# Kernel optimization log

Measured on AMD Instinct MI355X. Metric: run time of the kernel, lower is better.

Reference implementation:

```python
import jax, jax.numpy as jnp
import numpy as np
import math

B, N, D = 4096, 196, 32
M, H, W, NH = 12, 14, 14, 4
DH = D // NH


def _coords():
    # k_coords: (N,2) grid coords; q_coords: first M points of a (sqrt(M)+1)^2 linspace grid
    yy, xx = np.meshgrid(np.arange(H), np.arange(W), indexing='ij')
    k_coords = np.stack([yy.ravel(), xx.ravel()], axis=-1).astype(np.float32)
    g = int(math.sqrt(M)) + 1  # 4
    cy = np.linspace(0, H - 1, g)
    cx = np.linspace(0, W - 1, g)
    gy, gx = np.meshgrid(cy, cx, indexing='ij')
    grid = np.stack([gy.ravel(), gx.ravel()], axis=-1).astype(np.float32)
    q_coords = grid[:M]
    return jnp.asarray(q_coords), jnp.asarray(k_coords)


def setup_inputs() -> dict:
    key = jax.random.key(0)
    ks = jax.random.split(key, 8)
    q_coords, k_coords = _coords()
    return {
        'T': jax.random.normal(ks[0], (B, N, D), jnp.float32),
        'Q': jax.random.normal(ks[1], (M, D), jnp.float32) * 0.02,
        'Wq': jax.random.normal(ks[2], (D, D), jnp.float32) / math.sqrt(D),
        'Wk': jax.random.normal(ks[3], (D, D), jnp.float32) / math.sqrt(D),
        'Wv': jax.random.normal(ks[4], (D, D), jnp.float32) / math.sqrt(D),
        'Wp': jax.random.normal(ks[5], (D, M * D), jnp.float32) / math.sqrt(M * D),
        'bp': jnp.zeros((D,), jnp.float32),
        'rpb_bias': jax.random.normal(ks[6], (NH, 2 * H - 1, 2 * W - 1), jnp.float32) * 0.02,
        'q_coords': q_coords,
        'k_coords': k_coords,
    }


def reference(T, Q, Wq, Wk, Wv, Wp, bp, rpb_bias, q_coords, k_coords):
    # projections (torch Linear: x @ W^T)
    Qp = Q @ Wq.T                      # (M, D)
    K = T @ Wk.T                       # (B, N, D)
    V = T @ Wv.T                       # (B, N, D)
    Qh = Qp.reshape(M, NH, DH).transpose(1, 0, 2)          # (nh, M, Dh)
    Kh = K.reshape(B, N, NH, DH).transpose(0, 2, 1, 3)     # (B, nh, N, Dh)
    Vh = V.reshape(B, N, NH, DH).transpose(0, 2, 1, 3)     # (B, nh, N, Dh)

    content = jnp.einsum('hmd,bhnd->bhmn', Qh, Kh) / math.sqrt(DH)

    # gathered relative position bias: (nh, M, N)
    dy = q_coords[:, None, 0] - k_coords[None, :, 0]
    dx = q_coords[:, None, 1] - k_coords[None, :, 1]
    idx_y = jnp.clip(jnp.round(dy) + (H - 1), 0, 2 * H - 2).astype(jnp.int32)
    idx_x = jnp.clip(jnp.round(dx) + (W - 1), 0, 2 * W - 2).astype(jnp.int32)
    rpb = rpb_bias[:, idx_y, idx_x]

    logits = content + rpb[None]                            # (B, nh, M, N)
    A = jax.nn.softmax(logits, axis=-1)

    A_avg = A.mean(axis=1)                                  # (B, M, N)
    topk = max(1, int(0.05 * N))                            # 9
    topk_mass = jax.lax.top_k(A_avg, topk)[0].sum(-1)       # (B, M)

    P = jnp.clip(A, 1e-12, None)
    Hn = -(P * jnp.log(P)).sum(-1) / math.log(N)            # (B, nh, M)
    head_energy = (1.0 - Hn).transpose(0, 2, 1)             # (B, M, nh)

    S = jnp.einsum('bhmn,bhnd->bhmd', A, Vh).transpose(0, 2, 1, 3).reshape(B, M, D)
    Z = S.reshape(B, M * D) @ Wp.T + bp                     # (B, D)
    A_maps = A_avg.reshape(B, M, H, W)
    return Z, A_maps, head_energy, S, topk_mass
```

## Files before the change

kernel.cpp:

```cpp
#include <hip/hip_runtime.h>
#include <math.h>


typedef float f32x4 __attribute__((ext_vector_type(4)));
typedef float f32x2 __attribute__((ext_vector_type(2)));
typedef _Float16 h2  __attribute__((ext_vector_type(2)));
typedef _Float16 h4v __attribute__((ext_vector_type(4)));
typedef _Float16 h8  __attribute__((ext_vector_type(8)));
typedef __fp16 fp16x2 __attribute__((ext_vector_type(2)));

#define LOG2E 1.4426950408889634f

__device__ __forceinline__ h2 cvt_pk(float a, float b){
  fp16x2 r = __builtin_amdgcn_cvt_pkrtz(a, b);
  return __builtin_bit_cast(h2, r);
}

__device__ __forceinline__ float dot4(float4 a, float4 b){
  return a.x*b.x + a.y*b.y + a.z*b.z + a.w*b.w;
}

__device__ __forceinline__ void barrier_lds(){
  asm volatile("s_waitcnt lgkmcnt(0)" ::: "memory");
  __builtin_amdgcn_s_barrier();
  asm volatile("" ::: "memory");
}

template<int CTRL>
__device__ __forceinline__ int idpp(int x, int id){
  return __builtin_amdgcn_update_dpp(id, x, CTRL, 0xF, 0xF, false);
}
__device__ __forceinline__ int wimax_all(int x){
  const int ID = 0;
  x = max(x, idpp<0x111>(x, ID));
  x = max(x, idpp<0x112>(x, ID));
  x = max(x, idpp<0x114>(x, ID));
  x = max(x, idpp<0x118>(x, ID));
  x = max(x, idpp<0x142>(x, ID));
  x = max(x, idpp<0x143>(x, ID));
  return __builtin_amdgcn_readlane(x, 63);
}

__global__ void prologue_kernel(const float* __restrict__ Q, const float* __restrict__ Wq,
                                const float* __restrict__ Wk, const float* __restrict__ Wv,
                                const float* __restrict__ rpb,
                                const float* __restrict__ qc, const float* __restrict__ kc,
                                _Float16* __restrict__ G16, float* __restrict__ rpbc32,
                                float* __restrict__ Wvp)
{
  __shared__ float Qp[384];
  const int tid = threadIdx.x;
  const int bid = blockIdx.x;

  if (bid == 0){
    for (int i = tid; i < 384; i += 256){
      int m = i >> 5, d = i & 31;
      float a = 0.f;
      #pragma unroll
      for (int c = 0; c < 32; ++c) a += Q[m*32+c] * Wq[d*32+c];
      Qp[i] = a;
    }
    __syncthreads();
    const float s = 0.35355339059327373f * LOG2E;
    for (int i = tid; i < 1536; i += 256){
      int hm = i >> 5, c = i & 31;
      int hh = hm / 12, mm = hm - 12*hh;
      float a = 0.f;
      #pragma unroll
      for (int dh = 0; dh < 8; ++dh) a += Qp[mm*32 + hh*8 + dh] * Wk[(hh*8+dh)*32 + c];
      G16[i] = (_Float16)(a * s);
    }
  }
  if (bid == 1){
    for (int i = tid; i < 1024; i += 256){
      int d = i >> 5, cp = i & 31;
      Wvp[i] = Wv[d*32 + (cp>>1) + ((cp&1)<<4)];
    }
  }
  int i = bid*256 + tid;
  if (i < 9984){
    int mh = i / 208, n = i - mh*208;
    float v;
    if (n < 196){
      int hh = mh / 12, mm = mh - 12*hh;
      float dy = qc[2*mm]   - kc[2*n];
      float dx = qc[2*mm+1] - kc[2*n+1];
      int iy = (int)rintf(dy) + 13; iy = iy < 0 ? 0 : (iy > 26 ? 26 : iy);
      int ix = (int)rintf(dx) + 13; ix = ix < 0 ? 0 : (ix > 26 ? 26 : ix);
      v = rpb[hh*729 + iy*27 + ix];
    } else {
      v = -60000.0f;
    }
    rpbc32[i] = v * LOG2E;
  }
}

__device__ __forceinline__ int ttoff(int n, int c8){
  return (n>>2)*128 + ((c8>>1)<<6) + ((n&3)<<4) + ((c8&1)<<3);
}

#define TRRD(dst, base, off) \
  asm volatile("ds_read_b64_tr_b16 %0, %1 offset:" #off : "=v"(dst) : "v"(base))
#define SH8(a, b) __builtin_shufflevector(a, b, 0,1,2,3,4,5,6,7)

__global__ __launch_bounds__(256, 4) void fused_main(
    const float* __restrict__ T, const float* __restrict__ Wvp, const float* __restrict__ Wp,
    const float* __restrict__ bp, const _Float16* __restrict__ G16,
    const float* __restrict__ rpbc32, float* __restrict__ out)
{
  __shared__ __align__(128) char smem[39456];
  _Float16* TT = (_Float16*)smem;
  _Float16* As = (_Float16*)(smem + 13312);
  float*    U  = (float*)(smem + 32544);
  float*    Ss = (float*)smem;

  const int b    = blockIdx.x;
  const int tid  = threadIdx.x;
  const int lane = tid & 63;
  const int h    = tid >> 6;
  const int r15  = lane & 15;
  const int g    = lane >> 4;

  float* outZ = out;
  float* outA = out + 131072;
  float* outE = out + 9764864;
  float* outS = out + 9961472;
  float* outK = out + 11534336;

  const float* Tb = T + (size_t)b*6272;
  #pragma unroll
  for (int ii = 0; ii < 3; ++ii){
    int i = tid + ii*256;
    int n = i >> 2, c8 = i & 3;
    const f32x4* src = (const f32x4*)(Tb + n*32 + c8*8);
    f32x4 v0 = __builtin_nontemporal_load(src);
    f32x4 v1 = __builtin_nontemporal_load(src + 1);
    h2 p0 = cvt_pk(v0[0], v0[1]);
    h2 p1 = cvt_pk(v0[2], v0[3]);
    h2 p2 = cvt_pk(v1[0], v1[1]);
    h2 p3 = cvt_pk(v1[2], v1[3]);
    h4v lo = __builtin_shufflevector(p0, p1, 0,1,2,3);
    h4v hi = __builtin_shufflevector(p2, p3, 0,1,2,3);
    *(h8*)&TT[ttoff(n, c8)] = __builtin_shufflevector(lo, hi, 0,1,2,3,4,5,6,7);
  }
  if (tid < 64){
    int i = 768 + tid;
    int n = i >> 2, c8 = i & 3;
    h8 hv = {0,0,0,0,0,0,0,0};
    if (n < 196){
      const f32x4* src = (const f32x4*)(Tb + n*32 + c8*8);
      f32x4 v0 = __builtin_nontemporal_load(src);
      f32x4 v1 = __builtin_nontemporal_load(src + 1);
      h2 p0 = cvt_pk(v0[0], v0[1]);
      h2 p1 = cvt_pk(v0[2], v0[3]);
      h2 p2 = cvt_pk(v1[0], v1[1]);
      h2 p3 = cvt_pk(v1[2], v1[3]);
      h4v lo = __builtin_shufflevector(p0, p1, 0,1,2,3);
      h4v hi = __builtin_shufflevector(p2, p3, 0,1,2,3);
      hv = __builtin_shufflevector(lo, hi, 0,1,2,3,4,5,6,7);
    }
    *(h8*)&TT[ttoff(n, c8)] = hv;
  }
  if (tid < 2){
    h8 z = {0,0,0,0,0,0,0,0};
    *(h8*)&As[9600 + tid*8] = z;
  }

  const int mhB = h*12 + (r15 < 12 ? r15 : 11);
  h8 bfrag = *(const h8*)(G16 + mhB*32 + g*8);
  f32x4 acc[13];
  #pragma unroll
  for (int t = 0; t < 13; ++t)
    acc[t] = *(const f32x4*)(rpbc32 + mhB*208 + t*16 + g*4);
  barrier_lds();

  const int rowoff = ((r15>>2)*128) + ((r15&3)<<4) + ((g>>1)<<6) + ((g&1)<<3);
  #pragma unroll
  for (int t = 0; t < 13; ++t){
    h8 af = *(const h8*)&TT[rowoff + t*512];
    acc[t] = __builtin_amdgcn_mfma_f32_16x16x32_f16(af, bfrag, acc[t], 0, 0, 0);
  }

  float se = 0.f, te = 0.f;
  #pragma unroll
  for (int t = 0; t < 13; ++t){
    #pragma unroll
    for (int r = 0; r < 4; ++r){
      float x = acc[t][r];
      float e = __builtin_amdgcn_exp2f(x);
      se += e; te += x*e;
      acc[t][r] = e;
    }
  }
  se += __shfl_xor(se, 16); se += __shfl_xor(se, 32);
  te += __shfl_xor(te, 16); te += __shfl_xor(te, 32);
  const float inv = 1.f / se;
  if (r15 < 12){
    #pragma unroll
    for (int t = 0; t < 13; ++t){
      if (t == 12){
        if (g >= 2) continue;
      }
      h2 w0 = cvt_pk(acc[t][0]*inv, acc[t][1]*inv);
      h2 w1 = cvt_pk(acc[t][2]*inv, acc[t][3]*inv);
      *(h4v*)&As[mhB*200 + t*16 + g*4] = __builtin_shufflevector(w0, w1, 0,1,2,3);
    }
    if (g == 0){
      const float LOG2N_INV = 0.13132474f;
      outE[(size_t)b*48 + r15*4 + h] = 1.0f + (te*inv - __log2f(se)) * LOG2N_INV;
    }
  }
  barrier_lds();

  if (h < 3){
    f32x4 u0 = {0,0,0,0}, u1 = {0,0,0,0};
    const int arow = h*16 + r15;
    const _Float16* Ab = &As[arow*200 + g*8];
    h8 af0 = *(const h8*)(Ab);
    h8 af1 = *(const h8*)(Ab + 32);
    h8 af2 = *(const h8*)(Ab + 64);
    h8 af3 = *(const h8*)(Ab + 96);
    h8 af4 = *(const h8*)(Ab + 128);
    h8 af5 = *(const h8*)(Ab + 160);
    h4v afT = *(const h4v*)&As[arow*200 + 192 + g*4];
    unsigned A0 = (unsigned)(size_t)&TT[0] + (unsigned)(g*512 + r15*8);
    unsigned At = (unsigned)(size_t)&TT[0] + (unsigned)(12288 + g*256 + r15*8);
    h4v t00,t01,t02,t03, t10,t11,t12,t13, t20,t21,t22,t23,
        t30,t31,t32,t33, t40,t41,t42,t43, t50,t51,t52,t53, tt0,tt1;
    TRRD(t00, A0, 0);     TRRD(t01, A0, 256);   TRRD(t02, A0, 128);   TRRD(t03, A0, 384);
    TRRD(t10, A0, 2048);  TRRD(t11, A0, 2304);  TRRD(t12, A0, 2176);  TRRD(t13, A0, 2432);
    TRRD(t20, A0, 4096);  TRRD(t21, A0, 4352);  TRRD(t22, A0, 4224);  TRRD(t23, A0, 4480);
    TRRD(t30, A0, 6144);  TRRD(t31, A0, 6400);  TRRD(t32, A0, 6272);  TRRD(t33, A0, 6528);
    TRRD(t40, A0, 8192);  TRRD(t41, A0, 8448);  TRRD(t42, A0, 8320);  TRRD(t43, A0, 8576);
    TRRD(t50, A0, 10240); TRRD(t51, A0, 10496); TRRD(t52, A0, 10368); TRRD(t53, A0, 10624);
    TRRD(tt0, At, 0);     TRRD(tt1, At, 128);
    asm volatile("s_waitcnt lgkmcnt(0)" ::: "memory");
    __builtin_amdgcn_sched_barrier(0);
    u0 = __builtin_amdgcn_mfma_f32_16x16x32_f16(af0, SH8(t00,t01), u0, 0, 0, 0);
    u1 = __builtin_amdgcn_mfma_f32_16x16x32_f16(af0, SH8(t02,t03), u1, 0, 0, 0);
    u0 = __builtin_amdgcn_mfma_f32_16x16x32_f16(af1, SH8(t10,t11), u0, 0, 0, 0);
    u1 = __builtin_amdgcn_mfma_f32_16x16x32_f16(af1, SH8(t12,t13), u1, 0, 0, 0);
    u0 = __builtin_amdgcn_mfma_f32_16x16x32_f16(af2, SH8(t20,t21), u0, 0, 0, 0);
    u1 = __builtin_amdgcn_mfma_f32_16x16x32_f16(af2, SH8(t22,t23), u1, 0, 0, 0);
    u0 = __builtin_amdgcn_mfma_f32_16x16x32_f16(af3, SH8(t30,t31), u0, 0, 0, 0);
    u1 = __builtin_amdgcn_mfma_f32_16x16x32_f16(af3, SH8(t32,t33), u1, 0, 0, 0);
    u0 = __builtin_amdgcn_mfma_f32_16x16x32_f16(af4, SH8(t40,t41), u0, 0, 0, 0);
    u1 = __builtin_amdgcn_mfma_f32_16x16x32_f16(af4, SH8(t42,t43), u1, 0, 0, 0);
    u0 = __builtin_amdgcn_mfma_f32_16x16x32_f16(af5, SH8(t50,t51), u0, 0, 0, 0);
    u1 = __builtin_amdgcn_mfma_f32_16x16x32_f16(af5, SH8(t52,t53), u1, 0, 0, 0);
    u0 = __builtin_amdgcn_mfma_f32_16x16x16f16(afT, tt0, u0, 0, 0, 0);
    u1 = __builtin_amdgcn_mfma_f32_16x16x16f16(afT, tt1, u1, 0, 0, 0);
    #pragma unroll
    for (int r = 0; r < 4; ++r){
      f32x2 p = {u0[r], u1[r]};
      *(f32x2*)&U[(h*16 + g*4 + r)*36 + r15*2] = p;
    }
  }

  {
    const bool act = (lane < 49);
    const int nb4 = lane * 4;
    int K00=0,K01=0,K02=0,K03=0, K10=0,K11=0,K12=0,K13=0, K20=0,K21=0,K22=0,K23=0;
    float mass0=0.f, mass1=0.f, mass2=0.f;
    const int m0 = h, m1 = h+4, m2 = h+8;

    #pragma unroll
    for (int mi = 0; mi < 3; ++mi){
      int m = (mi==0) ? m0 : ((mi==1) ? m1 : m2);
      if (act){
        h4v s0 = *(const h4v*)&As[(     m)*200 + nb4];
        h4v s1 = *(const h4v*)&As[(12 + m)*200 + nb4];
        h4v s2 = *(const h4v*)&As[(24 + m)*200 + nb4];
        h4v s3 = *(const h4v*)&As[(36 + m)*200 + nb4];
        h4v sh = (s0 + s1) + (s2 + s3);
        float a0 = 0.25f*(float)sh[0], a1 = 0.25f*(float)sh[1];
        float a2 = 0.25f*(float)sh[2], a3 = 0.25f*(float)sh[3];
        float* amrow = outA + (size_t)b*2352 + m*196 + nb4;
        f32x2 o0 = {a0, a1}, o1 = {a2, a3};
        __builtin_nontemporal_store(o0, (f32x2*)amrow);
        __builtin_nontemporal_store(o1, (f32x2*)(amrow + 2));
        int kk0 = (__builtin_bit_cast(int, a0) & ~0xFF) | (lane << 2) | 0;
        int kk1 = (__builtin_bit_cast(int, a1) & ~0xFF) | (lane << 2) | 1;
        int kk2 = (__builtin_bit_cast(int, a2) & ~0xFF) | (lane << 2) | 2;
        int kk3 = (__builtin_bit_cast(int, a3) & ~0xFF) | (lane << 2) | 3;
        if (mi == 0){ K00=kk0; K01=kk1; K02=kk2; K03=kk3; }
        else if (mi == 1){ K10=kk0; K11=kk1; K12=kk2; K13=kk3; }
        else { K20=kk0; K21=kk1; K22=kk2; K23=kk3; }
      }
    }
    #pragma unroll
    for (int k = 0; k < 9; ++k){
      int g0 = wimax_all(max(max(K00,K01), max(K02,K03)));
      int g1 = wimax_all(max(max(K10,K11), max(K12,K13)));
      int g2 = wimax_all(max(max(K20,K21), max(K22,K23)));
      mass0 += __builtin_bit_cast(float, g0 & ~0xFF);
      mass1 += __builtin_bit_cast(float, g1 & ~0xFF);
      mass2 += __builtin_bit_cast(float, g2 & ~0xFF);
      if (lane == ((g0 >> 2) & 63)){
        int q = g0 & 3;
        if (q==0) K00=0; else if (q==1) K01=0; else if (q==2) K02=0; else K03=0;
      }
      if (lane == ((g1 >> 2) & 63)){
        int q = g1 & 3;
        if (q==0) K10=0; else if (q==1) K11=0; else if (q==2) K12=0; else K13=0;
      }
      if (lane == ((g2 >> 2) & 63)){
        int q = g2 & 3;
        if (q==0) K20=0; else if (q==1) K21=0; else if (q==2) K22=0; else K23=0;
      }
    }
    if (lane == 0){
      __builtin_nontemporal_store(mass0, outK + (size_t)b*12 + m0);
      __builtin_nontemporal_store(mass1, outK + (size_t)b*12 + m1);
      __builtin_nontemporal_store(mass2, outK + (size_t)b*12 + m2);
    }
  }
  barrier_lds();

  for (int md = tid; md < 384; md += 256){
    int m = md >> 5, d = md & 31, hh = d >> 3;
    const float4* Urow = (const float4*)(U + (hh*12 + m)*36);
    const float4* Wvr  = (const float4*)(Wvp + d*32);
    float a = 0.f;
    #pragma unroll
    for (int q = 0; q < 8; ++q) a += dot4(Urow[q], Wvr[q]);
    Ss[md] = a;
    __builtin_nontemporal_store(a, outS + (size_t)b*384 + md);
  }
  barrier_lds();

  {
    int d = tid >> 3, j4 = tid & 7;
    const float4* Wp4 = (const float4*)(Wp + d*384);
    const float4* Ss4 = (const float4*)Ss;
    float a = 0.f;
    #pragma unroll
    for (int jj = 0; jj < 12; ++jj){
      int j = j4 + jj*8;
      a += dot4(Wp4[j], Ss4[j]);
    }
    a += __shfl_xor(a, 1);
    a += __shfl_xor(a, 2);
    a += __shfl_xor(a, 4);
    if (j4 == 0)
      __builtin_nontemporal_store(bp[d] + a, outZ + (size_t)b*32 + d);
  }
}

extern "C" void kernel_launch(void* const* d_in, const int* in_sizes, int n_in,
                              void* d_out, int out_size, void* d_ws, size_t ws_size,
                              hipStream_t stream)
{
  const float* T    = (const float*)d_in[0];
  const float* Q    = (const float*)d_in[1];
  const float* Wq   = (const float*)d_in[2];
  const float* Wk   = (const float*)d_in[3];
  const float* Wv   = (const float*)d_in[4];
  const float* Wp   = (const float*)d_in[5];
  const float* bp   = (const float*)d_in[6];
  const float* rpb  = (const float*)d_in[7];
  const float* qc   = (const float*)d_in[8];
  const float* kc   = (const float*)d_in[9];
  _Float16* G16  = (_Float16*)d_ws;
  float* rpbc32  = (float*)((char*)d_ws + 4096);
  float* Wvp     = (float*)((char*)d_ws + 44032);
  float* outp = (float*)d_out;

  prologue_kernel<<<40, 256, 0, stream>>>(Q, Wq, Wk, Wv, rpb, qc, kc, G16, rpbc32, Wvp);
  fused_main<<<4096, 256, 0, stream>>>(T, Wvp, Wp, bp, G16, rpbc32, outp);
}
```

Before: 69.37 us.

## Make fused kernel persistent over four batches with register-prefetched next tile

The grid shrinks from one block per batch to 1024 blocks, each looping over four batch elements. During each iteration the next batch's T tile is loaded from global memory into registers while the top-k and output phases run, then packed into LDS after a barrier. Ss moves to a separate LDS region so it does not collide with the TT tile being refilled. This aims to hide global load latency and amortize block launch, but it raises register pressure and gives fewer blocks to balance across CUs.

After: 198.4 us. 2.86x slower.

```diff
diff --git a/kernel.cpp b/kernel.cpp
--- a/kernel.cpp
+++ b/kernel.cpp
@@ -10,10 +10,19 @@
 typedef __fp16 fp16x2 __attribute__((ext_vector_type(2)));
 
 #define LOG2E 1.4426950408889634f
+#define GRIDB 1024
+#define NB    4
 
 __device__ __forceinline__ h2 cvt_pk(float a, float b){
   fp16x2 r = __builtin_amdgcn_cvt_pkrtz(a, b);
   return __builtin_bit_cast(h2, r);
+}
+__device__ __forceinline__ h8 pack8(f32x4 a, f32x4 b){
+  h2 q0 = cvt_pk(a[0],a[1]), q1 = cvt_pk(a[2],a[3]);
+  h2 q2 = cvt_pk(b[0],b[1]), q3 = cvt_pk(b[2],b[3]);
+  h4v lo = __builtin_shufflevector(q0,q1,0,1,2,3);
+  h4v hi = __builtin_shufflevector(q2,q3,0,1,2,3);
+  return __builtin_shufflevector(lo,hi,0,1,2,3,4,5,6,7);
 }
 
 __device__ __forceinline__ float dot4(float4 a, float4 b){
@@ -112,9 +121,9 @@
   _Float16* TT = (_Float16*)smem;
   _Float16* As = (_Float16*)(smem + 13312);
   float*    U  = (float*)(smem + 32544);
-  float*    Ss = (float*)smem;
-
-  const int b    = blockIdx.x;
+  float*    Ss = (float*)(smem + 13312);
+
+  const int bid  = blockIdx.x;
   const int tid  = threadIdx.x;
   const int lane = tid & 63;
   const int h    = tid >> 6;
@@ -127,39 +136,28 @@
   float* outS = out + 9961472;
   float* outK = out + 11534336;
 
-  const float* Tb = T + (size_t)b*6272;
-  #pragma unroll
-  for (int ii = 0; ii < 3; ++ii){
-    int i = tid + ii*256;
-    int n = i >> 2, c8 = i & 3;
-    const f32x4* src = (const f32x4*)(Tb + n*32 + c8*8);
-    f32x4 v0 = __builtin_nontemporal_load(src);
-    f32x4 v1 = __builtin_nontemporal_load(src + 1);
-    h2 p0 = cvt_pk(v0[0], v0[1]);
-    h2 p1 = cvt_pk(v0[2], v0[3]);
-    h2 p2 = cvt_pk(v1[0], v1[1]);
-    h2 p3 = cvt_pk(v1[2], v1[3]);
-    h4v lo = __builtin_shufflevector(p0, p1, 0,1,2,3);
-    h4v hi = __builtin_shufflevector(p2, p3, 0,1,2,3);
-    *(h8*)&TT[ttoff(n, c8)] = __builtin_shufflevector(lo, hi, 0,1,2,3,4,5,6,7);
-  }
-  if (tid < 64){
-    int i = 768 + tid;
-    int n = i >> 2, c8 = i & 3;
-    h8 hv = {0,0,0,0,0,0,0,0};
-    if (n < 196){
-      const f32x4* src = (const f32x4*)(Tb + n*32 + c8*8);
+  {
+    const float* Tb = T + (size_t)bid*6272;
+    #pragma unroll
+    for (int ii = 0; ii < 3; ++ii){
+      int i = tid + ii*256;
+      const f32x4* src = (const f32x4*)(Tb + (i>>2)*32 + (i&3)*8);
       f32x4 v0 = __builtin_nontemporal_load(src);
       f32x4 v1 = __builtin_nontemporal_load(src + 1);
-      h2 p0 = cvt_pk(v0[0], v0[1]);
-      h2 p1 = cvt_pk(v0[2], v0[3]);
-      h2 p2 = cvt_pk(v1[0], v1[1]);
-      h2 p3 = cvt_pk(v1[2], v1[3]);
-      h4v lo = __builtin_shufflevector(p0, p1, 0,1,2,3);
-      h4v hi = __builtin_shufflevector(p2, p3, 0,1,2,3);
-      hv = __builtin_shufflevector(lo, hi, 0,1,2,3,4,5,6,7);
-    }
-    *(h8*)&TT[ttoff(n, c8)] = hv;
+      *(h8*)&TT[ttoff(i>>2, i&3)] = pack8(v0, v1);
+    }
+    if (tid < 64){
+      int i = 768 + tid;
+      int n = i >> 2;
+      h8 hv = {0,0,0,0,0,0,0,0};
+      if (n < 196){
+        const f32x4* src = (const f32x4*)(Tb + n*32 + (i&3)*8);
+        f32x4 v0 = __builtin_nontemporal_load(src);
+        f32x4 v1 = __builtin_nontemporal_load(src + 1);
+        hv = pack8(v0, v1);
+      }
+      *(h8*)&TT[ttoff(n, i&3)] = hv;
+    }
   }
   if (tid < 2){
     h8 z = {0,0,0,0,0,0,0,0};
@@ -167,183 +165,230 @@
   }
 
   const int mhB = h*12 + (r15 < 12 ? r15 : 11);
-  h8 bfrag = *(const h8*)(G16 + mhB*32 + g*8);
+  const h8 bfrag = *(const h8*)(G16 + mhB*32 + g*8);
   f32x4 acc[13];
   #pragma unroll
   for (int t = 0; t < 13; ++t)
     acc[t] = *(const f32x4*)(rpbc32 + mhB*208 + t*16 + g*4);
-  barrier_lds();
 
   const int rowoff = ((r15>>2)*128) + ((r15&3)<<4) + ((g>>1)<<6) + ((g&1)<<3);
-  #pragma unroll
-  for (int t = 0; t < 13; ++t){
-    h8 af = *(const h8*)&TT[rowoff + t*512];
-    acc[t] = __builtin_amdgcn_mfma_f32_16x16x32_f16(af, bfrag, acc[t], 0, 0, 0);
-  }
-
-  float se = 0.f, te = 0.f;
-  #pragma unroll
-  for (int t = 0; t < 13; ++t){
-    #pragma unroll
-    for (int r = 0; r < 4; ++r){
-      float x = acc[t][r];
-      float e = __builtin_amdgcn_exp2f(x);
-      se += e; te += x*e;
-      acc[t][r] = e;
-    }
-  }
-  se += __shfl_xor(se, 16); se += __shfl_xor(se, 32);
-  te += __shfl_xor(te, 16); te += __shfl_xor(te, 32);
-  const float inv = 1.f / se;
-  if (r15 < 12){
+
+  for (int it = 0; it < NB; ++it){
+    const int b = bid + it*GRIDB;
+    barrier_lds();
+
     #pragma unroll
     for (int t = 0; t < 13; ++t){
-      if (t == 12){
-        if (g >= 2) continue;
-      }
-      h2 w0 = cvt_pk(acc[t][0]*inv, acc[t][1]*inv);
-      h2 w1 = cvt_pk(acc[t][2]*inv, acc[t][3]*inv);
-      *(h4v*)&As[mhB*200 + t*16 + g*4] = __builtin_shufflevector(w0, w1, 0,1,2,3);
-    }
-    if (g == 0){
-      const float LOG2N_INV = 0.13132474f;
-      outE[(size_t)b*48 + r15*4 + h] = 1.0f + (te*inv - __log2f(se)) * LOG2N_INV;
-    }
-  }
-  barrier_lds();
-
-  if (h < 3){
-    f32x4 u0 = {0,0,0,0}, u1 = {0,0,0,0};
-    const int arow = h*16 + r15;
-    const _Float16* Ab = &As[arow*200 + g*8];
-    h8 af0 = *(const h8*)(Ab);
-    h8 af1 = *(const h8*)(Ab + 32);
-    h8 af2 = *(const h8*)(Ab + 64);
-    h8 af3 = *(const h8*)(Ab + 96);
-    h8 af4 = *(const h8*)(Ab + 128);
-    h8 af5 = *(const h8*)(Ab + 160);
-    h4v afT = *(const h4v*)&As[arow*200 + 192 + g*4];
-    unsigned A0 = (unsigned)(size_t)&TT[0] + (unsigned)(g*512 + r15*8);
-    unsigned At = (unsigned)(size_t)&TT[0] + (unsigned)(12288 + g*256 + r15*8);
-    h4v t00,t01,t02,t03, t10,t11,t12,t13, t20,t21,t22,t23,
-        t30,t31,t32,t33, t40,t41,t42,t43, t50,t51,t52,t53, tt0,tt1;
-    TRRD(t00, A0, 0);     TRRD(t01, A0, 256);   TRRD(t02, A0, 128);   TRRD(t03, A0, 384);
-    TRRD(t10, A0, 2048);  TRRD(t11, A0, 2304);  TRRD(t12, A0, 2176);  TRRD(t13, A0, 2432);
-    TRRD(t20, A0, 4096);  TRRD(t21, A0, 4352);  TRRD(t22, A0, 4224);  TRRD(t23, A0, 4480);
-    TRRD(t30, A0, 6144);  TRRD(t31, A0, 6400);  TRRD(t32, A0, 6272);  TRRD(t33, A0, 6528);
-    TRRD(t40, A0, 8192);  TRRD(t41, A0, 8448);  TRRD(t42, A0, 8320);  TRRD(t43, A0, 8576);
-    TRRD(t50, A0, 10240); TRRD(t51, A0, 10496); TRRD(t52, A0, 10368); TRRD(t53, A0, 10624);
-    TRRD(tt0, At, 0);     TRRD(tt1, At, 128);
-    asm volatile("s_waitcnt lgkmcnt(0)" ::: "memory");
-    __builtin_amdgcn_sched_barrier(0);
-    u0 = __builtin_amdgcn_mfma_f32_16x16x32_f16(af0, SH8(t00,t01), u0, 0, 0, 0);
-    u1 = __builtin_amdgcn_mfma_f32_16x16x32_f16(af0, SH8(t02,t03), u1, 0, 0, 0);
-    u0 = __builtin_amdgcn_mfma_f32_16x16x32_f16(af1, SH8(t10,t11), u0, 0, 0, 0);
-    u1 = __builtin_amdgcn_mfma_f32_16x16x32_f16(af1, SH8(t12,t13), u1, 0, 0, 0);
-    u0 = __builtin_amdgcn_mfma_f32_16x16x32_f16(af2, SH8(t20,t21), u0, 0, 0, 0);
-    u1 = __builtin_amdgcn_mfma_f32_16x16x32_f16(af2, SH8(t22,t23), u1, 0, 0, 0);
-    u0 = __builtin_amdgcn_mfma_f32_16x16x32_f16(af3, SH8(t30,t31), u0, 0, 0, 0);
-    u1 = __builtin_amdgcn_mfma_f32_16x16x32_f16(af3, SH8(t32,t33), u1, 0, 0, 0);
-    u0 = __builtin_amdgcn_mfma_f32_16x16x32_f16(af4, SH8(t40,t41), u0, 0, 0, 0);
-    u1 = __builtin_amdgcn_mfma_f32_16x16x32_f16(af4, SH8(t42,t43), u1, 0, 0, 0);
-    u0 = __builtin_amdgcn_mfma_f32_16x16x32_f16(af5, SH8(t50,t51), u0, 0, 0, 0);
-    u1 = __builtin_amdgcn_mfma_f32_16x16x32_f16(af5, SH8(t52,t53), u1, 0, 0, 0);
-    u0 = __builtin_amdgcn_mfma_f32_16x16x16f16(afT, tt0, u0, 0, 0, 0);
-    u1 = __builtin_amdgcn_mfma_f32_16x16x16f16(afT, tt1, u1, 0, 0, 0);
+      h8 af = *(const h8*)&TT[rowoff + t*512];
+      acc[t] = __builtin_amdgcn_mfma_f32_16x16x32_f16(af, bfrag, acc[t], 0, 0, 0);
+    }
+
+    float se = 0.f, te = 0.f;
     #pragma unroll
-    for (int r = 0; r < 4; ++r){
-      f32x2 p = {u0[r], u1[r]};
-      *(f32x2*)&U[(h*16 + g*4 + r)*36 + r15*2] = p;
-    }
-  }
-
-  {
-    const bool act = (lane < 49);
-    const int nb4 = lane * 4;
-    int K00=0,K01=0,K02=0,K03=0, K10=0,K11=0,K12=0,K13=0, K20=0,K21=0,K22=0,K23=0;
-    float mass0=0.f, mass1=0.f, mass2=0.f;
-    const int m0 = h, m1 = h+4, m2 = h+8;
-
-    #pragma unroll
-    for (int mi = 0; mi < 3; ++mi){
-      int m = (mi==0) ? m0 : ((mi==1) ? m1 : m2);
-      if (act){
-        h4v s0 = *(const h4v*)&As[(     m)*200 + nb4];
-        h4v s1 = *(const h4v*)&As[(12 + m)*200 + nb4];
-        h4v s2 = *(const h4v*)&As[(24 + m)*200 + nb4];
-        h4v s3 = *(const h4v*)&As[(36 + m)*200 + nb4];
-        h4v sh = (s0 + s1) + (s2 + s3);
-        float a0 = 0.25f*(float)sh[0], a1 = 0.25f*(float)sh[1];
-        float a2 = 0.25f*(float)sh[2], a3 = 0.25f*(float)sh[3];
-        float* amrow = outA + (size_t)b*2352 + m*196 + nb4;
-        f32x2 o0 = {a0, a1}, o1 = {a2, a3};
-        __builtin_nontemporal_store(o0, (f32x2*)amrow);
-        __builtin_nontemporal_store(o1, (f32x2*)(amrow + 2));
-        int kk0 = (__builtin_bit_cast(int, a0) & ~0xFF) | (lane << 2) | 0;
-        int kk1 = (__builtin_bit_cast(int, a1) & ~0xFF) | (lane << 2) | 1;
-        int kk2 = (__builtin_bit_cast(int, a2) & ~0xFF) | (lane << 2) | 2;
-        int kk3 = (__builtin_bit_cast(int, a3) & ~0xFF) | (lane << 2) | 3;
-        if (mi == 0){ K00=kk0; K01=kk1; K02=kk2; K03=kk3; }
-        else if (mi == 1){ K10=kk0; K11=kk1; K12=kk2; K13=kk3; }
-        else { K20=kk0; K21=kk1; K22=kk2; K23=kk3; }
-      }
-    }
-    #pragma unroll
-    for (int k = 0; k < 9; ++k){
-      int g0 = wimax_all(max(max(K00,K01), max(K02,K03)));
-      int g1 = wimax_all(max(max(K10,K11), max(K12,K13)));
-      int g2 = wimax_all(max(max(K20,K21), max(K22,K23)));
-      mass0 += __builtin_bit_cast(float, g0 & ~0xFF);
-      mass1 += __builtin_bit_cast(float, g1 & ~0xFF);
-      mass2 += __builtin_bit_cast(float, g2 & ~0xFF);
-      if (lane == ((g0 >> 2) & 63)){
-        int q = g0 & 3;
-        if (q==0) K00=0; else if (q==1) K01=0; else if (q==2) K02=0; else K03=0;
-      }
-      if (lane == ((g1 >> 2) & 63)){
-        int q = g1 & 3;
-        if (q==0) K10=0; else if (q==1) K11=0; else if (q==2) K12=0; else K13=0;
-      }
-      if (lane == ((g2 >> 2) & 63)){
-        int q = g2 & 3;
-        if (q==0) K20=0; else if (q==1) K21=0; else if (q==2) K22=0; else K23=0;
-      }
-    }
-    if (lane == 0){
-      __builtin_nontemporal_store(mass0, outK + (size_t)b*12 + m0);
-      __builtin_nontemporal_store(mass1, outK + (size_t)b*12 + m1);
-      __builtin_nontemporal_store(mass2, outK + (size_t)b*12 + m2);
-    }
-  }
-  barrier_lds();
-
-  for (int md = tid; md < 384; md += 256){
-    int m = md >> 5, d = md & 31, hh = d >> 3;
-    const float4* Urow = (const float4*)(U + (hh*12 + m)*36);
-    const float4* Wvr  = (const float4*)(Wvp + d*32);
-    float a = 0.f;
-    #pragma unroll
-    for (int q = 0; q < 8; ++q) a += dot4(Urow[q], Wvr[q]);
-    Ss[md] = a;
-    __builtin_nontemporal_store(a, outS + (size_t)b*384 + md);
-  }
-  barrier_lds();
-
-  {
-    int d = tid >> 3, j4 = tid & 7;
-    const float4* Wp4 = (const float4*)(Wp + d*384);
-    const float4* Ss4 = (const float4*)Ss;
-    float a = 0.f;
-    #pragma unroll
-    for (int jj = 0; jj < 12; ++jj){
-      int j = j4 + jj*8;
-      a += dot4(Wp4[j], Ss4[j]);
-    }
-    a += __shfl_xor(a, 1);
-    a += __shfl_xor(a, 2);
-    a += __shfl_xor(a, 4);
-    if (j4 == 0)
-      __builtin_nontemporal_store(bp[d] + a, outZ + (size_t)b*32 + d);
+    for (int t = 0; t < 13; ++t){
+      #pragma unroll
+      for (int r = 0; r < 4; ++r){
+        float x = acc[t][r];
+        float e = __builtin_amdgcn_exp2f(x);
+        se += e; te += x*e;
+        acc[t][r] = e;
+      }
+    }
+    se += __shfl_xor(se, 16); se += __shfl_xor(se, 32);
+    te += __shfl_xor(te, 16); te += __shfl_xor(te, 32);
+    const float inv = 1.f / se;
+    if (r15 < 12){
+      #pragma unroll
+      for (int t = 0; t < 13; ++t){
+        if (t == 12){
+          if (g >= 2) continue;
+        }
+        h2 w0 = cvt_pk(acc[t][0]*inv, acc[t][1]*inv);
+        h2 w1 = cvt_pk(acc[t][2]*inv, acc[t][3]*inv);
+        *(h4v*)&As[mhB*200 + t*16 + g*4] = __builtin_shufflevector(w0, w1, 0,1,2,3);
+      }
+      if (g == 0){
+        const float LOG2N_INV = 0.13132474f;
+        outE[(size_t)b*48 + r15*4 + h] = 1.0f + (te*inv - __log2f(se)) * LOG2N_INV;
+      }
+    }
+    barrier_lds();
+
+    if (h < 3){
+      f32x4 u0 = {0,0,0,0}, u1 = {0,0,0,0};
+      const int arow = h*16 + r15;
+      const _Float16* Ab = &As[arow*200 + g*8];
+      h8 af0 = *(const h8*)(Ab);
+      h8 af1 = *(const h8*)(Ab + 32);
+      h8 af2 = *(const h8*)(Ab + 64);
+      h8 af3 = *(const h8*)(Ab + 96);
+      h8 af4 = *(const h8*)(Ab + 128);
+      h8 af5 = *(const h8*)(Ab + 160);
+      h4v afT = *(const h4v*)&As[arow*200 + 192 + g*4];
+      unsigned A0 = (unsigned)(size_t)&TT[0] + (unsigned)(g*512 + r15*8);
+      unsigned At = (unsigned)(size_t)&TT[0] + (unsigned)(12288 + g*256 + r15*8);
+      h4v t00,t01,t02,t03, t10,t11,t12,t13, t20,t21,t22,t23,
+          t30,t31,t32,t33, t40,t41,t42,t43, t50,t51,t52,t53, tt0,tt1;
+      TRRD(t00, A0, 0);     TRRD(t01, A0, 256);   TRRD(t02, A0, 128);   TRRD(t03, A0, 384);
+      TRRD(t10, A0, 2048);  TRRD(t11, A0, 2304);  TRRD(t12, A0, 2176);  TRRD(t13, A0, 2432);
+      TRRD(t20, A0, 4096);  TRRD(t21, A0, 4352);  TRRD(t22, A0, 4224);  TRRD(t23, A0, 4480);
+      TRRD(t30, A0, 6144);  TRRD(t31, A0, 6400);  TRRD(t32, A0, 6272);  TRRD(t33, A0, 6528);
+      TRRD(t40, A0, 8192);  TRRD(t41, A0, 8448);  TRRD(t42, A0, 8320);  TRRD(t43, A0, 8576);
+      TRRD(t50, A0, 10240); TRRD(t51, A0, 10496); TRRD(t52, A0, 10368); TRRD(t53, A0, 10624);
+      TRRD(tt0, At, 0);     TRRD(tt1, At, 128);
+      asm volatile("s_waitcnt lgkmcnt(0)" ::: "memory");
+      __builtin_amdgcn_sched_barrier(0);
+      u0 = __builtin_amdgcn_mfma_f32_16x16x32_f16(af0, SH8(t00,t01), u0, 0, 0, 0);
+      u1 = __builtin_amdgcn_mfma_f32_16x16x32_f16(af0, SH8(t02,t03), u1, 0, 0, 0);
+      u0 = __builtin_amdgcn_mfma_f32_16x16x32_f16(af1, SH8(t10,t11), u0, 0, 0, 0);
+      u1 = __builtin_amdgcn_mfma_f32_16x16x32_f16(af1, SH8(t12,t13), u1, 0, 0, 0);
+      u0 = __builtin_amdgcn_mfma_f32_16x16x32_f16(af2, SH8(t20,t21), u0, 0, 0, 0);
+      u1 = __builtin_amdgcn_mfma_f32_16x16x32_f16(af2, SH8(t22,t23), u1, 0, 0, 0);
+      u0 = __builtin_amdgcn_mfma_f32_16x16x32_f16(af3, SH8(t30,t31), u0, 0, 0, 0);
+      u1 = __builtin_amdgcn_mfma_f32_16x16x32_f16(af3, SH8(t32,t33), u1, 0, 0, 0);
+      u0 = __builtin_amdgcn_mfma_f32_16x16x32_f16(af4, SH8(t40,t41), u0, 0, 0, 0);
+      u1 = __builtin_amdgcn_mfma_f32_16x16x32_f16(af4, SH8(t42,t43), u1, 0, 0, 0);
+      u0 = __builtin_amdgcn_mfma_f32_16x16x32_f16(af5, SH8(t50,t51), u0, 0, 0, 0);
+      u1 = __builtin_amdgcn_mfma_f32_16x16x32_f16(af5, SH8(t52,t53), u1, 0, 0, 0);
+      u0 = __builtin_amdgcn_mfma_f32_16x16x16f16(afT, tt0, u0, 0, 0, 0);
+      u1 = __builtin_amdgcn_mfma_f32_16x16x16f16(afT, tt1, u1, 0, 0, 0);
+      #pragma unroll
+      for (int r = 0; r < 4; ++r){
+        f32x2 p = {u0[r], u1[r]};
+        *(f32x2*)&U[(h*16 + g*4 + r)*36 + r15*2] = p;
+      }
+    }
+
+    f32x4 p0a,p0b,p1a,p1b,p2a,p2b;
+    f32x4 p3a = {0,0,0,0}, p3b = {0,0,0,0};
+    if (it < NB-1){
+      const float* Tn = T + (size_t)(b + GRIDB)*6272;
+      {
+        const f32x4* s = (const f32x4*)(Tn + (tid>>2)*32 + (tid&3)*8);
+        p0a = __builtin_nontemporal_load(s); p0b = __builtin_nontemporal_load(s+1);
+      }
+      {
+        int i = tid + 256;
+        const f32x4* s = (const f32x4*)(Tn + (i>>2)*32 + (i&3)*8);
+        p1a = __builtin_nontemporal_load(s); p1b = __builtin_nontemporal_load(s+1);
+      }
+      {
+        int i = tid + 512;
+        const f32x4* s = (const f32x4*)(Tn + (i>>2)*32 + (i&3)*8);
+        p2a = __builtin_nontemporal_load(s); p2b = __builtin_nontemporal_load(s+1);
+      }
+      if (tid < 64){
+        int i = 768 + tid; int n = i >> 2;
+        if (n < 196){
+          const f32x4* s = (const f32x4*)(Tn + n*32 + (i&3)*8);
+          p3a = __builtin_nontemporal_load(s); p3b = __builtin_nontemporal_load(s+1);
+        }
+      }
+    }
+
+    {
+      const bool act = (lane < 49);
+      const int nb4 = lane * 4;
+      int K00=0,K01=0,K02=0,K03=0, K10=0,K11=0,K12=0,K13=0, K20=0,K21=0,K22=0,K23=0;
+      float mass0=0.f, mass1=0.f, mass2=0.f;
+      const int m0 = h, m1 = h+4, m2 = h+8;
+
+      #pragma unroll
+      for (int mi = 0; mi < 3; ++mi){
+        int m = (mi==0) ? m0 : ((mi==1) ? m1 : m2);
+        if (act){
+          h4v s0 = *(const h4v*)&As[(     m)*200 + nb4];
+          h4v s1 = *(const h4v*)&As[(12 + m)*200 + nb4];
+          h4v s2 = *(const h4v*)&As[(24 + m)*200 + nb4];
+          h4v s3 = *(const h4v*)&As[(36 + m)*200 + nb4];
+          h4v sh = (s0 + s1) + (s2 + s3);
+          float a0 = 0.25f*(float)sh[0], a1 = 0.25f*(float)sh[1];
+          float a2 = 0.25f*(float)sh[2], a3 = 0.25f*(float)sh[3];
+          float* amrow = outA + (size_t)b*2352 + m*196 + nb4;
+          f32x2 o0 = {a0, a1}, o1 = {a2, a3};
+          __builtin_nontemporal_store(o0, (f32x2*)amrow);
+          __builtin_nontemporal_store(o1, (f32x2*)(amrow + 2));
+          int kk0 = (__builtin_bit_cast(int, a0) & ~0xFF) | (lane << 2) | 0;
+          int kk1 = (__builtin_bit_cast(int, a1) & ~0xFF) | (lane << 2) | 1;
+          int kk2 = (__builtin_bit_cast(int, a2) & ~0xFF) | (lane << 2) | 2;
+          int kk3 = (__builtin_bit_cast(int, a3) & ~0xFF) | (lane << 2) | 3;
+          if (mi == 0){ K00=kk0; K01=kk1; K02=kk2; K03=kk3; }
+          else if (mi == 1){ K10=kk0; K11=kk1; K12=kk2; K13=kk3; }
+          else { K20=kk0; K21=kk1; K22=kk2; K23=kk3; }
+        }
+      }
+      #pragma unroll
+      for (int k = 0; k < 9; ++k){
+        int g0 = wimax_all(max(max(K00,K01), max(K02,K03)));
+        int g1 = wimax_all(max(max(K10,K11), max(K12,K13)));
+        int g2 = wimax_all(max(max(K20,K21), max(K22,K23)));
+        mass0 += __builtin_bit_cast(float, g0 & ~0xFF);
+        mass1 += __builtin_bit_cast(float, g1 & ~0xFF);
+        mass2 += __builtin_bit_cast(float, g2 & ~0xFF);
+        if (lane == ((g0 >> 2) & 63)){
+          int q = g0 & 3;
+          if (q==0) K00=0; else if (q==1) K01=0; else if (q==2) K02=0; else K03=0;
+        }
+        if (lane == ((g1 >> 2) & 63)){
+          int q = g1 & 3;
+          if (q==0) K10=0; else if (q==1) K11=0; else if (q==2) K12=0; else K13=0;
+        }
+        if (lane == ((g2 >> 2) & 63)){
+          int q = g2 & 3;
+          if (q==0) K20=0; else if (q==1) K21=0; else if (q==2) K22=0; else K23=0;
+        }
+      }
+      if (lane == 0){
+        __builtin_nontemporal_store(mass0, outK + (size_t)b*12 + m0);
+        __builtin_nontemporal_store(mass1, outK + (size_t)b*12 + m1);
+        __builtin_nontemporal_store(mass2, outK + (size_t)b*12 + m2);
+      }
+    }
+    barrier_lds();
+
+    if (it < NB-1){
+      *(h8*)&TT[ttoff(tid>>2, tid&3)] = pack8(p0a, p0b);
+      { int i = tid+256; *(h8*)&TT[ttoff(i>>2, i&3)] = pack8(p1a, p1b); }
+      { int i = tid+512; *(h8*)&TT[ttoff(i>>2, i&3)] = pack8(p2a, p2b); }
+      if (tid < 64){
+        int i = 768 + tid; int n = i >> 2;
+        h8 hv = {0,0,0,0,0,0,0,0};
+        if (n < 196) hv = pack8(p3a, p3b);
+        *(h8*)&TT[ttoff(n, i&3)] = hv;
+      }
+      #pragma unroll
+      for (int t = 0; t < 13; ++t)
+        acc[t] = *(const f32x4*)(rpbc32 + mhB*208 + t*16 + g*4);
+    }
+
+    for (int md = tid; md < 384; md += 256){
+      int m = md >> 5, d = md & 31, hh = d >> 3;
+      const float4* Urow = (const float4*)(U + (hh*12 + m)*36);
+      const float4* Wvr  = (const float4*)(Wvp + d*32);
+      float a = 0.f;
+      #pragma unroll
+      for (int q = 0; q < 8; ++q) a += dot4(Urow[q], Wvr[q]);
+      Ss[md] = a;
+      __builtin_nontemporal_store(a, outS + (size_t)b*384 + md);
+    }
+    barrier_lds();
+
+    {
+      int d = tid >> 3, j4 = tid & 7;
+      const float4* Wp4 = (const float4*)(Wp + d*384);
+      const float4* Ss4 = (const float4*)Ss;
+      float a = 0.f;
+      #pragma unroll
+      for (int jj = 0; jj < 12; ++jj){
+        int j = j4 + jj*8;
+        a += dot4(Wp4[j], Ss4[j]);
+      }
+      a += __shfl_xor(a, 1);
+      a += __shfl_xor(a, 2);
+      a += __shfl_xor(a, 4);
+      if (j4 == 0)
+        __builtin_nontemporal_store(bp[d] + a, outZ + (size_t)b*32 + d);
+    }
   }
 }
 
@@ -367,5 +412,5 @@
   float* outp = (float*)d_out;
 
   prologue_kernel<<<40, 256, 0, stream>>>(Q, Wq, Wk, Wv, rpb, qc, kc, G16, rpbc32, Wvp);
-  fused_main<<<4096, 256, 0, stream>>>(T, Wvp, Wp, bp, G16, rpbc32, outp);
-}
+  fused_main<<<GRIDB, 256, 0, stream>>>(T, Wvp, Wp, bp, G16, rpbc32, outp);
+}
```
